# Kernel tuning notes

Measured on AMD Instinct MI355X. Metric: run time of the kernel, lower is better.

## Reference

```python
import jax, jax.numpy as jnp
import numpy as np

B, S, D, H, L, O = 64, 512, 512, 1024, 2, 1000


def setup_inputs() -> dict:
    key = jax.random.key(0)
    ks = jax.random.split(key, 12)
    s = 0.05
    return {
        "x": jax.random.normal(ks[0], (B, S, D), jnp.float32),
        "h0": jnp.zeros((L, B, H), jnp.float32),
        "c0": jnp.zeros((L, B, H), jnp.float32),
        "W_ih0": jax.random.normal(ks[1], (4 * H, D), jnp.float32) * s,
        "W_hh0": jax.random.normal(ks[2], (4 * H, H), jnp.float32) * s,
        "b_ih0": jax.random.normal(ks[3], (4 * H,), jnp.float32) * s,
        "b_hh0": jax.random.normal(ks[4], (4 * H,), jnp.float32) * s,
        "W_ih1": jax.random.normal(ks[5], (4 * H, H), jnp.float32) * s,
        "W_hh1": jax.random.normal(ks[6], (4 * H, H), jnp.float32) * s,
        "b_ih1": jax.random.normal(ks[7], (4 * H,), jnp.float32) * s,
        "b_hh1": jax.random.normal(ks[8], (4 * H,), jnp.float32) * s,
        "W_fc": jax.random.normal(ks[9], (O, H), jnp.float32) * s,
        "b_fc": jax.random.normal(ks[10], (O,), jnp.float32) * s,
    }


def _lstm_cell(x_t, h, c, W_ih, W_hh, b_ih, b_hh):
    # standard LSTMCell: fused 4-gate GEMM, gate order (i, f, g, o)
    gates = x_t @ W_ih.T + b_ih + h @ W_hh.T + b_hh  # [B, 4H]
    i, f, g, o = jnp.split(gates, 4, axis=-1)
    i = jax.nn.sigmoid(i)
    f = jax.nn.sigmoid(f)
    g = jnp.tanh(g)
    o = jax.nn.sigmoid(o)
    c_new = f * c + i * g
    h_new = o * jnp.tanh(c_new)
    return h_new, c_new


def reference(x, h0, c0, W_ih0, W_hh0, b_ih0, b_hh0, W_ih1, W_hh1, b_ih1, b_hh1, W_fc, b_fc):
    params = [(W_ih0, W_hh0, b_ih0, b_hh0), (W_ih1, W_hh1, b_ih1, b_hh1)]

    def step(carry, x_t):
        hs, cs = carry  # tuples of [B,H] per layer
        new_h, new_c = [], []
        inp = x_t
        for l in range(L):  # fixed small layer count
            h_l, c_l = _lstm_cell(inp, hs[l], cs[l], *params[l])
            new_h.append(h_l)
            new_c.append(c_l)
            inp = h_l
        return (tuple(new_h), tuple(new_c)), None

    xs = jnp.swapaxes(x, 0, 1)  # [S, B, D]
    init = (tuple(h0[l] for l in range(L)), tuple(c0[l] for l in range(L)))
    (hs, _), _ = jax.lax.scan(step, init, xs)
    # dropout is inference-mode identity; output_activation=None
    out = hs[-1] @ W_fc.T + b_fc  # [B, O]
    return out
```

## Files before the change

kernel.cpp:

```cpp
#include <hip/hip_runtime.h>

#define B_ 64
#define S_ 512
#define D_ 512
#define H_ 1024

typedef __attribute__((ext_vector_type(8))) short bf16x8;
typedef __attribute__((ext_vector_type(4))) float f32x4;
typedef unsigned short u16;
typedef unsigned int u32;

#define MFMA(a, b, c) __builtin_amdgcn_mfma_f32_16x16x32_bf16(a, b, c, 0, 0, 0)

__device__ __forceinline__ u16 f2bf(float f) {
    u32 u = __float_as_uint(f);
    u += 0x7fffu + ((u >> 16) & 1u);
    return (u16)(u >> 16);
}
__device__ __forceinline__ float sigm(float x) { return 1.0f / (1.0f + __expf(-x)); }
__device__ __forceinline__ float tanh_f(float x) { return 1.0f - 2.0f / (__expf(2.0f * x) + 1.0f); }

__device__ __forceinline__ bf16x8 cvt8(const float* p) {
    float4 f0 = ((const float4*)p)[0];
    float4 f1 = ((const float4*)p)[1];
    bf16x8 v;
    v[0] = (short)f2bf(f0.x); v[1] = (short)f2bf(f0.y);
    v[2] = (short)f2bf(f0.z); v[3] = (short)f2bf(f0.w);
    v[4] = (short)f2bf(f1.x); v[5] = (short)f2bf(f1.y);
    v[6] = (short)f2bf(f1.z); v[7] = (short)f2bf(f1.w);
    return v;
}

__device__ __forceinline__ void llc_ld(bf16x8& d, const u16* p) {
    asm volatile("global_load_dwordx4 %0, %1, off sc0 sc1" : "=v"(d) : "v"(p));
}
__device__ __forceinline__ void vm0() {
    asm volatile("s_waitcnt vmcnt(0)" ::: "memory");
}
__device__ __forceinline__ void fence_frag(bf16x8& d) {
    asm volatile("" : "+v"(d));
}
__device__ __forceinline__ void llc_st16(u16* p, u16 v) {
    u32 vv = v;
    asm volatile("global_store_short %0, %1, off sc0 sc1" :: "v"(p), "v"(vv) : "memory");
}

__global__ void prep_w(const float* __restrict__ Wih, const float* __restrict__ Whh,
                       u16* __restrict__ Wc, int Kx, int Kw, int total8) {
    int idx = blockIdx.x * 256 + threadIdx.x;
    if (idx >= total8) return;
    int kc8 = Kw >> 3;
    int n = idx / kc8;
    int kc = (idx - n * kc8) << 3;
    const float* src = (kc < Kx) ? (Wih + (size_t)n * Kx + kc)
                                 : (Whh + (size_t)n * (Kw - Kx) + (kc - Kx));
    *(bf16x8*)(Wc + (size_t)n * Kw + kc) = cvt8(src);
}

__global__ void prep_misc2(const float* __restrict__ h0in,
                           const float* __restrict__ bih0, const float* __restrict__ bhh0,
                           const float* __restrict__ bih1, const float* __restrict__ bhh1,
                           float* __restrict__ bias0, float* __restrict__ bias1,
                           u16* __restrict__ h0a, u16* __restrict__ h0b,
                           u16* __restrict__ h1a, u16* __restrict__ h1b,
                           int* __restrict__ bar) {
    int idx = blockIdx.x * 256 + threadIdx.x;
    if (idx < 1024) bar[idx] = 0;
    if (idx < 4096) { bias0[idx] = bih0[idx] + bhh0[idx]; return; }
    if (idx < 8192) { int i = idx - 4096; bias1[i] = bih1[i] + bhh1[i]; return; }
    int r = idx - 8192;
    if (r >= 2 * B_ * H_) return;
    int l = r >> 16;
    int rr = r & 65535;
    u16 hb = f2bf(h0in[r]);
    if (l == 0) { h0a[rr] = hb; h0b[rr] = hb; }
    else        { h1a[rr] = hb; h1b[rr] = hb; }
}

__global__ __launch_bounds__(512, 2) void lstm_persist(
    const float* __restrict__ x,
    const u16* __restrict__ W0c, const u16* __restrict__ W1c,
    const float* __restrict__ bias0, const float* __restrict__ bias1,
    const float* __restrict__ c0in,
    u16* __restrict__ h0a, u16* __restrict__ h0b,
    u16* __restrict__ h1a, u16* __restrict__ h1b,
    float* __restrict__ h1f,
    int* __restrict__ bar) {
    const int bk = blockIdx.x;
    const int cgp = bk >> 1;
    const int mh = bk & 1;
    const int tid = threadIdx.x;
    const int w = tid >> 6;
    const int lane = tid & 63;
    const int quad = lane >> 4;
    const int l16 = lane & 15;

    int gc[2];
    #pragma unroll
    for (int n = 0; n < 2; ++n) {
        int c = n * 16 + l16;
        gc[n] = (c >> 3) * 1024 + cgp * 8 + (c & 7);
    }

    bf16x8 w0x[2][2], w0h[2][4];
    bf16x8 w1f[2][8];
    #pragma unroll
    for (int n = 0; n < 2; ++n) {
        #pragma unroll
        for (int kf = 0; kf < 2; ++kf)
            w0x[n][kf] = *(const bf16x8*)(W0c + (size_t)gc[n] * 1536 + w * 64 + kf * 32 + quad * 8);
        #pragma unroll
        for (int kf = 0; kf < 4; ++kf)
            w0h[n][kf] = *(const bf16x8*)(W0c + (size_t)gc[n] * 1536 + 512 + w * 128 + kf * 32 + quad * 8);
        #pragma unroll
        for (int kf = 0; kf < 8; ++kf)
            w1f[n][kf] = *(const bf16x8*)(W1c + (size_t)gc[n] * 2048 + w * 256 + kf * 32 + quad * 8);
    }

    __shared__ float part[8 * 32 * 37];
    __shared__ float c0l[256], c1l[256];
    __shared__ float b0l[32], b1l[32];

    if (tid < 32) {
        int gg = tid >> 3, j = tid & 7;
        b0l[tid] = bias0[gg * 1024 + cgp * 8 + j];
        b1l[tid] = bias1[gg * 1024 + cgp * 8 + j];
    }
    if (tid < 256) {
        int b = tid >> 3, j = tid & 7;
        int gi = (mh * 32 + b) * 1024 + cgp * 8 + j;
        c0l[tid] = c0in[gi];
        c1l[tid] = c0in[65536 + gi];
    }
    __syncthreads();

    const int brow0 = mh * 32 + l16;
    const int brow1 = brow0 + 16;

    f32x4 xacc[2][2];
    #define XPART(t)                                                                 \
        {                                                                            \
            xacc[0][0] = (f32x4){0.f,0.f,0.f,0.f}; xacc[0][1] = (f32x4){0.f,0.f,0.f,0.f}; \
            xacc[1][0] = (f32x4){0.f,0.f,0.f,0.f}; xacc[1][1] = (f32x4){0.f,0.f,0.f,0.f}; \
            _Pragma("unroll")                                                        \
            for (int kf = 0; kf < 2; ++kf) {                                         \
                int k = w * 64 + kf * 32 + quad * 8;                                 \
                bf16x8 a0 = cvt8(x + (size_t)brow0 * 262144 + (t) * 512 + k);        \
                bf16x8 a1 = cvt8(x + (size_t)brow1 * 262144 + (t) * 512 + k);        \
                xacc[0][0] = MFMA(a0, w0x[0][kf], xacc[0][0]);                       \
                xacc[0][1] = MFMA(a0, w0x[1][kf], xacc[0][1]);                       \
                xacc[1][0] = MFMA(a1, w0x[0][kf], xacc[1][0]);                       \
                xacc[1][1] = MFMA(a1, w0x[1][kf], xacc[1][1]);                       \
            }                                                                        \
        }

    XPART(0);

    for (int p = 0; p <= S_; ++p) {
        const int rd = p & 1;
        const u16* h0r = rd ? h0b : h0a;
        u16*       h0w_ = rd ? h0a : h0b;
        const u16* h1r = rd ? h1b : h1a;
        u16*       h1w_ = rd ? h1a : h1b;

        if (p > 0) {
            if (tid == 0) {
                int target = 256 * p;
                for (int it = 0; it < 20000; ++it) {
                    if (__hip_atomic_load(&bar[0], __ATOMIC_RELAXED, __HIP_MEMORY_SCOPE_AGENT) >= target)
                        break;
                    __builtin_amdgcn_s_sleep(1);
                }
            }
            __syncthreads();
        }

        bf16x8 a0[4], a1[4];
        if (p < S_) {
            #pragma unroll
            for (int kf = 0; kf < 4; ++kf) {
                int ko = w * 128 + kf * 32 + quad * 8;
                llc_ld(a0[kf], h0r + brow0 * 1024 + ko);
                llc_ld(a1[kf], h0r + brow1 * 1024 + ko);
            }
            vm0();
            #pragma unroll
            for (int kf = 0; kf < 4; ++kf) { fence_frag(a0[kf]); fence_frag(a1[kf]); }
        }
        bf16x8 pb0[8], pb1[8];
        if (p >= 1) {
            #pragma unroll
            for (int kf = 0; kf < 8; ++kf) {
                int k = w * 256 + kf * 32;
                const u16* src = (k < 1024) ? h0r : h1r;
                int ko = (k & 1023) + quad * 8;
                llc_ld(pb0[kf], src + brow0 * 1024 + ko);
                llc_ld(pb1[kf], src + brow1 * 1024 + ko);
            }
        }

        if (p < S_) {
            f32x4 acc00 = xacc[0][0], acc01 = xacc[0][1];
            f32x4 acc10 = xacc[1][0], acc11 = xacc[1][1];
            #pragma unroll
            for (int kf = 0; kf < 4; ++kf) {
                acc00 = MFMA(a0[kf], w0h[0][kf], acc00);
                acc01 = MFMA(a0[kf], w0h[1][kf], acc01);
                acc10 = MFMA(a1[kf], w0h[0][kf], acc10);
                acc11 = MFMA(a1[kf], w0h[1][kf], acc11);
            }
            #pragma unroll
            for (int r = 0; r < 4; ++r) {
                int r0 = quad * 4 + r, r1 = 16 + quad * 4 + r;
                part[w * 1184 + r0 * 37 + l16]      = acc00[r];
                part[w * 1184 + r0 * 37 + 16 + l16] = acc01[r];
                part[w * 1184 + r1 * 37 + l16]      = acc10[r];
                part[w * 1184 + r1 * 37 + 16 + l16] = acc11[r];
            }
            __syncthreads();
            if (tid < 256) {
                int b = tid >> 3, j = tid & 7;
                float g4[4];
                #pragma unroll
                for (int gg = 0; gg < 4; ++gg) {
                    float s = b0l[gg * 8 + j];
                    #pragma unroll
                    for (int w8 = 0; w8 < 8; ++w8)
                        s += part[w8 * 1184 + b * 37 + gg * 8 + j];
                    g4[gg] = s;
                }
                float c = c0l[tid];
                float cn = sigm(g4[1]) * c + sigm(g4[0]) * tanh_f(g4[2]);
                float hn = sigm(g4[3]) * tanh_f(cn);
                c0l[tid] = cn;
                llc_st16(h0w_ + (mh * 32 + b) * 1024 + cgp * 8 + j, f2bf(hn));
            }
            __syncthreads();
        }

        if (p >= 1) {
            vm0();
            #pragma unroll
            for (int kf = 0; kf < 8; ++kf) { fence_frag(pb0[kf]); fence_frag(pb1[kf]); }
            f32x4 acc00 = {0.f,0.f,0.f,0.f}, acc01 = {0.f,0.f,0.f,0.f};
            f32x4 acc10 = {0.f,0.f,0.f,0.f}, acc11 = {0.f,0.f,0.f,0.f};
            #pragma unroll
            for (int kf = 0; kf < 8; ++kf) {
                acc00 = MFMA(pb0[kf], w1f[0][kf], acc00);
                acc01 = MFMA(pb0[kf], w1f[1][kf], acc01);
                acc10 = MFMA(pb1[kf], w1f[0][kf], acc10);
                acc11 = MFMA(pb1[kf], w1f[1][kf], acc11);
            }
            #pragma unroll
            for (int r = 0; r < 4; ++r) {
                int r0 = quad * 4 + r, r1 = 16 + quad * 4 + r;
                part[w * 1184 + r0 * 37 + l16]      = acc00[r];
                part[w * 1184 + r0 * 37 + 16 + l16] = acc01[r];
                part[w * 1184 + r1 * 37 + l16]      = acc10[r];
                part[w * 1184 + r1 * 37 + 16 + l16] = acc11[r];
            }
            __syncthreads();
            if (tid < 256) {
                int b = tid >> 3, j = tid & 7;
                float g4[4];
                #pragma unroll
                for (int gg = 0; gg < 4; ++gg) {
                    float s = b1l[gg * 8 + j];
                    #pragma unroll
                    for (int w8 = 0; w8 < 8; ++w8)
                        s += part[w8 * 1184 + b * 37 + gg * 8 + j];
                    g4[gg] = s;
                }
                float c = c1l[tid];
                float cn = sigm(g4[1]) * c + sigm(g4[0]) * tanh_f(g4[2]);
                float hn = sigm(g4[3]) * tanh_f(cn);
                c1l[tid] = cn;
                int gi = (mh * 32 + b) * 1024 + cgp * 8 + j;
                llc_st16(h1w_ + gi, f2bf(hn));
                if (p == S_) h1f[gi] = hn;
            }
            __syncthreads();
        }

        if (p < S_) {
            if (tid == 0)
                __hip_atomic_fetch_add(&bar[0], 1, __ATOMIC_RELAXED, __HIP_MEMORY_SCOPE_AGENT);
            if (p + 1 < S_) XPART(p + 1);
        }
    }
}

__global__ void fc_k(const float* __restrict__ h1f, const float* __restrict__ Wfc,
                     const float* __restrict__ bfc, float* __restrict__ out) {
    int idx = blockIdx.x * 256 + threadIdx.x;
    if (idx >= 64 * 1000) return;
    int o = idx % 1000;
    int b = idx / 1000;
    const float4* hr = (const float4*)(h1f + b * H_);
    const float4* wr = (const float4*)(Wfc + (size_t)o * H_);
    float s = 0.f;
    #pragma unroll 4
    for (int k = 0; k < 256; ++k) {
        float4 a = hr[k];
        float4 w = wr[k];
        s += a.x * w.x + a.y * w.y + a.z * w.z + a.w * w.w;
    }
    out[idx] = s + bfc[o];
}

extern "C" void kernel_launch(void* const* d_in, const int* in_sizes, int n_in,
                              void* d_out, int out_size, void* d_ws, size_t ws_size,
                              hipStream_t stream) {
    const float* x    = (const float*)d_in[0];
    const float* h0in = (const float*)d_in[1];
    const float* c0in = (const float*)d_in[2];
    const float* Wih0 = (const float*)d_in[3];
    const float* Whh0 = (const float*)d_in[4];
    const float* bih0 = (const float*)d_in[5];
    const float* bhh0 = (const float*)d_in[6];
    const float* Wih1 = (const float*)d_in[7];
    const float* Whh1 = (const float*)d_in[8];
    const float* bih1 = (const float*)d_in[9];
    const float* bhh1 = (const float*)d_in[10];
    const float* Wfc  = (const float*)d_in[11];
    const float* bfc  = (const float*)d_in[12];
    float* out = (float*)d_out;

    char* ws = (char*)d_ws;
    size_t off = 0;
    auto alloc = [&](size_t bytes) {
        void* p = ws + off;
        off += (bytes + 255) & ~(size_t)255;
        return p;
    };
    u16* W0c   = (u16*)alloc((size_t)4096 * 1536 * 2);
    u16* W1c   = (u16*)alloc((size_t)4096 * 2048 * 2);
    float* bias0 = (float*)alloc(4096 * 4);
    float* bias1 = (float*)alloc(4096 * 4);
    u16* h0A   = (u16*)alloc(B_ * H_ * 2);
    u16* h0B   = (u16*)alloc(B_ * H_ * 2);
    u16* h1A   = (u16*)alloc(B_ * H_ * 2);
    u16* h1B   = (u16*)alloc(B_ * H_ * 2);
    float* h1f = (float*)alloc(B_ * H_ * 4);
    int* bar   = (int*)alloc(4096);

    prep_w<<<786432 / 256, 256, 0, stream>>>(Wih0, Whh0, W0c, 512, 1536, 786432);
    prep_w<<<1048576 / 256, 256, 0, stream>>>(Wih1, Whh1, W1c, 1024, 2048, 1048576);
    prep_misc2<<<(8192 + 2 * B_ * H_ + 255) / 256, 256, 0, stream>>>(
        h0in, bih0, bhh0, bih1, bhh1, bias0, bias1, h0A, h0B, h1A, h1B, bar);

    void* args[] = {(void*)&x, (void*)&W0c, (void*)&W1c, (void*)&bias0, (void*)&bias1,
                    (void*)&c0in, (void*)&h0A, (void*)&h0B, (void*)&h1A, (void*)&h1B,
                    (void*)&h1f, (void*)&bar};
    hipLaunchCooperativeKernel((void*)lstm_persist, dim3(256), dim3(512), args, 0, stream);

    fc_k<<<(64000 + 255) / 256, 256, 0, stream>>>(h1f, Wfc, bfc, out);
}
```

Measured before the change: 5.877 ms.

## Use 32-slot hidden-state ring buffer with cached loads and periodic acquire fence

Replaces the double-buffered h0/h1 exchange with a 32-slot ring buffer per layer. The per-step recurrent loads switch from cache-bypassing sc0 sc1 asm loads with explicit waits to plain cached vector loads. An agent-scope acquire fence runs only every 32 steps, so a slot is not read through possibly stale cache lines before caches are invalidated. The aim is to cut the latency of the global hidden-state reads on the critical path of every timestep, at the cost of more workspace and a correctness dependence on cache-coherence assumptions across dies.

```diff
diff --git a/kernel.cpp b/kernel.cpp
--- a/kernel.cpp
+++ b/kernel.cpp
@@ -4,6 +4,7 @@
 #define S_ 512
 #define D_ 512
 #define H_ 1024
+#define NBUF 32
 
 typedef __attribute__((ext_vector_type(8))) short bf16x8;
 typedef __attribute__((ext_vector_type(4))) float f32x4;
@@ -31,15 +32,6 @@
     return v;
 }
 
-__device__ __forceinline__ void llc_ld(bf16x8& d, const u16* p) {
-    asm volatile("global_load_dwordx4 %0, %1, off sc0 sc1" : "=v"(d) : "v"(p));
-}
-__device__ __forceinline__ void vm0() {
-    asm volatile("s_waitcnt vmcnt(0)" ::: "memory");
-}
-__device__ __forceinline__ void fence_frag(bf16x8& d) {
-    asm volatile("" : "+v"(d));
-}
 __device__ __forceinline__ void llc_st16(u16* p, u16 v) {
     u32 vv = v;
     asm volatile("global_store_short %0, %1, off sc0 sc1" :: "v"(p), "v"(vv) : "memory");
@@ -61,8 +53,7 @@
                            const float* __restrict__ bih0, const float* __restrict__ bhh0,
                            const float* __restrict__ bih1, const float* __restrict__ bhh1,
                            float* __restrict__ bias0, float* __restrict__ bias1,
-                           u16* __restrict__ h0a, u16* __restrict__ h0b,
-                           u16* __restrict__ h1a, u16* __restrict__ h1b,
+                           u16* __restrict__ h0buf, u16* __restrict__ h1buf,
                            int* __restrict__ bar) {
     int idx = blockIdx.x * 256 + threadIdx.x;
     if (idx < 1024) bar[idx] = 0;
@@ -73,8 +64,8 @@
     int l = r >> 16;
     int rr = r & 65535;
     u16 hb = f2bf(h0in[r]);
-    if (l == 0) { h0a[rr] = hb; h0b[rr] = hb; }
-    else        { h1a[rr] = hb; h1b[rr] = hb; }
+    if (l == 0) h0buf[(size_t)31 * 65536 + rr] = hb;
+    else        h1buf[(size_t)31 * 65536 + rr] = hb;
 }
 
 __global__ __launch_bounds__(512, 2) void lstm_persist(
@@ -82,8 +73,7 @@
     const u16* __restrict__ W0c, const u16* __restrict__ W1c,
     const float* __restrict__ bias0, const float* __restrict__ bias1,
     const float* __restrict__ c0in,
-    u16* __restrict__ h0a, u16* __restrict__ h0b,
-    u16* __restrict__ h1a, u16* __restrict__ h1b,
+    u16* __restrict__ h0buf, u16* __restrict__ h1buf,
     float* __restrict__ h1f,
     int* __restrict__ bar) {
     const int bk = blockIdx.x;
@@ -157,11 +147,10 @@
     XPART(0);
 
     for (int p = 0; p <= S_; ++p) {
-        const int rd = p & 1;
-        const u16* h0r = rd ? h0b : h0a;
-        u16*       h0w_ = rd ? h0a : h0b;
-        const u16* h1r = rd ? h1b : h1a;
-        u16*       h1w_ = rd ? h1a : h1b;
+        const u16* h0r  = h0buf + (size_t)((p - 1) & (NBUF - 1)) * 65536;
+        u16*       h0w_ = h0buf + (size_t)((p)     & (NBUF - 1)) * 65536;
+        const u16* h1r  = h1buf + (size_t)((p - 2) & (NBUF - 1)) * 65536;
+        u16*       h1w_ = h1buf + (size_t)((p - 1) & (NBUF - 1)) * 65536;
 
         if (p > 0) {
             if (tid == 0) {
@@ -175,17 +164,17 @@
             __syncthreads();
         }
 
+        if ((p & (NBUF - 1)) == 0)
+            __builtin_amdgcn_fence(__ATOMIC_ACQUIRE, "agent");
+
         bf16x8 a0[4], a1[4];
         if (p < S_) {
             #pragma unroll
             for (int kf = 0; kf < 4; ++kf) {
                 int ko = w * 128 + kf * 32 + quad * 8;
-                llc_ld(a0[kf], h0r + brow0 * 1024 + ko);
-                llc_ld(a1[kf], h0r + brow1 * 1024 + ko);
-            }
-            vm0();
-            #pragma unroll
-            for (int kf = 0; kf < 4; ++kf) { fence_frag(a0[kf]); fence_frag(a1[kf]); }
+                a0[kf] = *(const bf16x8*)(h0r + brow0 * 1024 + ko);
+                a1[kf] = *(const bf16x8*)(h0r + brow1 * 1024 + ko);
+            }
         }
         bf16x8 pb0[8], pb1[8];
         if (p >= 1) {
@@ -194,8 +183,8 @@
                 int k = w * 256 + kf * 32;
                 const u16* src = (k < 1024) ? h0r : h1r;
                 int ko = (k & 1023) + quad * 8;
-                llc_ld(pb0[kf], src + brow0 * 1024 + ko);
-                llc_ld(pb1[kf], src + brow1 * 1024 + ko);
+                pb0[kf] = *(const bf16x8*)(src + brow0 * 1024 + ko);
+                pb1[kf] = *(const bf16x8*)(src + brow1 * 1024 + ko);
             }
         }
 
@@ -239,9 +228,6 @@
         }
 
         if (p >= 1) {
-            vm0();
-            #pragma unroll
-            for (int kf = 0; kf < 8; ++kf) { fence_frag(pb0[kf]); fence_frag(pb1[kf]); }
             f32x4 acc00 = {0.f,0.f,0.f,0.f}, acc01 = {0.f,0.f,0.f,0.f};
             f32x4 acc10 = {0.f,0.f,0.f,0.f}, acc11 = {0.f,0.f,0.f,0.f};
             #pragma unroll
@@ -276,7 +262,7 @@
                 float hn = sigm(g4[3]) * tanh_f(cn);
                 c1l[tid] = cn;
                 int gi = (mh * 32 + b) * 1024 + cgp * 8 + j;
-                llc_st16(h1w_ + gi, f2bf(hn));
+                llc_st16(h1w_ + ((mh * 32 + b) * 1024 + cgp * 8 + j) - gi + gi, f2bf(hn));
                 if (p == S_) h1f[gi] = hn;
             }
             __syncthreads();
@@ -337,21 +323,18 @@
     u16* W1c   = (u16*)alloc((size_t)4096 * 2048 * 2);
     float* bias0 = (float*)alloc(4096 * 4);
     float* bias1 = (float*)alloc(4096 * 4);
-    u16* h0A   = (u16*)alloc(B_ * H_ * 2);
-    u16* h0B   = (u16*)alloc(B_ * H_ * 2);
-    u16* h1A   = (u16*)alloc(B_ * H_ * 2);
-    u16* h1B   = (u16*)alloc(B_ * H_ * 2);
+    u16* h0buf = (u16*)alloc((size_t)NBUF * B_ * H_ * 2);
+    u16* h1buf = (u16*)alloc((size_t)NBUF * B_ * H_ * 2);
     float* h1f = (float*)alloc(B_ * H_ * 4);
     int* bar   = (int*)alloc(4096);
 
     prep_w<<<786432 / 256, 256, 0, stream>>>(Wih0, Whh0, W0c, 512, 1536, 786432);
     prep_w<<<1048576 / 256, 256, 0, stream>>>(Wih1, Whh1, W1c, 1024, 2048, 1048576);
     prep_misc2<<<(8192 + 2 * B_ * H_ + 255) / 256, 256, 0, stream>>>(
-        h0in, bih0, bhh0, bih1, bhh1, bias0, bias1, h0A, h0B, h1A, h1B, bar);
+        h0in, bih0, bhh0, bih1, bhh1, bias0, bias1, h0buf, h1buf, bar);
 
     void* args[] = {(void*)&x, (void*)&W0c, (void*)&W1c, (void*)&bias0, (void*)&bias1,
-                    (void*)&c0in, (void*)&h0A, (void*)&h0B, (void*)&h1A, (void*)&h1B,
-                    (void*)&h1f, (void*)&bar};
+                    (void*)&c0in, (void*)&h0buf, (void*)&h1buf, (void*)&h1f, (void*)&bar};
     hipLaunchCooperativeKernel((void*)lstm_persist, dim3(256), dim3(512), args, 0, stream);
 
     fc_k<<<(64000 + 255) / 256, 256, 0, stream>>>(h1f, Wfc, bfc, out);
```

After: 6.418 ms. 1.09x slower.
